# Performance work log

Hardware: AMD Instinct MI355X
Metric: run time of the kernel (lower is better)

The kernel has to match this reference:

```python
import jax, jax.numpy as jnp
import numpy as np

ALPHA = 0.2

def _ema_last_weights(T, alpha, dtype):
    # Closed form for the final EMA value after the sequential recurrence:
    # ema_T = (1-a)^(T-1) * x_0 + sum_{t=1}^{T-1} a*(1-a)^(T-1-t) * x_t
    t = jnp.arange(T)
    w = alpha * (1.0 - alpha) ** (T - 1 - t)
    w = w.at[0].set((1.0 - alpha) ** (T - 1))
    return w.astype(dtype)


def setup_inputs() -> dict:
    key = jax.random.key(0)
    k1, k2 = jax.random.split(key)
    B, T, F = 64, 2048, 256
    x = jax.random.normal(k1, (B, T, F), dtype=jnp.float32)
    W = jax.random.normal(k2, (F, F), dtype=jnp.float32) * (1.0 / np.sqrt(F))
    b = jnp.zeros((F,), dtype=jnp.float32)
    return {"x": x, "W": W, "b": b}


def reference(x, W, b):
    B, T, F = x.shape
    # final-step EMA over time (equivalent to the sequential python loop)
    w = _ema_last_weights(T, ALPHA, x.dtype)          # [T]
    last_ref = jnp.einsum('t,btf->bf', w, x)[:, None, :]  # [B,1,F]
    # base residual predictor: per-timestep linear
    res = jnp.einsum('btf,fg->btg', x, W) + b          # [B,T,F]
    return last_ref + res
```

## Files before the change

kernel.cpp:

```cpp
#include <hip/hip_runtime.h>

#define Bdim 64
#define Tdim 2048
#define Fdim 256
#define TAIL 256
#define NCH 8
#define CHT 32

#define NCHUNK 8
#define FR_STR 520

typedef __bf16 bf16x8 __attribute__((ext_vector_type(8)));
typedef float f32x16 __attribute__((ext_vector_type(16)));
typedef unsigned short u16x8 __attribute__((ext_vector_type(8)));

__device__ __forceinline__ unsigned short bf16_rne(float f) {
  unsigned int u = __float_as_uint(f);
  u += 0x7FFFu + ((u >> 16) & 1u);
  return (unsigned short)(u >> 16);
}

__global__ void prep(const float* __restrict__ x, const float* __restrict__ W,
                     unsigned short* __restrict__ Wf, float* __restrict__ part) {
  int blk = blockIdx.x;
  if (blk < Fdim) {
    int o = blk * 256 + threadIdx.x;
    int e = o & 7, lane = (o >> 3) & 63, wh = (o >> 9) & 1, s = (o >> 10) & 1;
    int c = (o >> 11) & 7, w = o >> 14;
    int n = w * 64 + wh * 32 + (lane & 31);
    int k = c * 32 + (2 * s + (lane >> 5)) * 8 + e;
    Wf[o] = bf16_rne(W[k * Fdim + n]);
  } else {
    int j = blk - Fdim;
    int b = j & 63, c = j >> 6;
    int f = threadIdx.x;
    int t0 = Tdim - TAIL + c * CHT;
    float w = 0.2f * exp2f((float)(Tdim - 1 - t0) * -0.32192809488736235f);
    const float* xp = x + ((size_t)b * Tdim + t0) * Fdim + f;
    float s = 0.f;
#pragma unroll
    for (int q = 0; q < CHT; ++q) {
      s += w * xp[(size_t)q * Fdim];
      w *= 1.25f;
    }
    part[(c * Bdim + b) * Fdim + f] = s;
  }
}

__global__ __launch_bounds__(256, 3)
void gemm_fused(const float* __restrict__ x, const unsigned short* __restrict__ Wf,
                const float* __restrict__ bias, const float* __restrict__ part,
                float* __restrict__ out) {
  __shared__ unsigned short Afrag[32 * FR_STR];
  __shared__ float lref[Fdim];

  const int tid = threadIdx.x;
  const int blk = blockIdx.x;
  const int b = blk >> 5;
  const size_t row0 = (size_t)blk * 64;

  const int wave = tid >> 6;
  const int lane = tid & 63;
  const int lm = lane & 31;
  const int half = lane >> 5;

  const int r = tid >> 2, q = tid & 3;
  const int iw = r >> 5;
  const int sq = q >> 1, hb = q & 1;
  const int dl = hb * 32 + (r & 31);
  const int wpos = dl ^ ((dl >> 5) << 2);
  const float* ap = x + (row0 + r) * Fdim + q * 8;

  float4 av[8][2];
#pragma unroll
  for (int p = 0; p < 8; ++p) {
    av[p][0] = *(const float4*)(ap + p * 32);
    av[p][1] = *(const float4*)(ap + p * 32 + 4);
  }

  {
    float s = bias[tid];
#pragma unroll
    for (int c = 0; c < NCH; ++c) s += part[(c * Bdim + b) * Fdim + tid];
    lref[tid] = s;
  }

#pragma unroll
  for (int p = 0; p < 8; ++p) {
    float4 v0 = av[p][0], v1 = av[p][1];
    u16x8 w;
    w[0] = bf16_rne(v0.x); w[1] = bf16_rne(v0.y);
    w[2] = bf16_rne(v0.z); w[3] = bf16_rne(v0.w);
    w[4] = bf16_rne(v1.x); w[5] = bf16_rne(v1.y);
    w[6] = bf16_rne(v1.z); w[7] = bf16_rne(v1.w);
    const int fragidx = (p * 2 + iw) * 2 + sq;
    *(u16x8*)&Afrag[fragidx * FR_STR + wpos * 8] = w;
  }
  __syncthreads();

  const unsigned short* bx = Wf + (size_t)wave * (32 * 512) + lane * 8;
  const int rpos = lane ^ ((lane >> 5) << 2);
  const unsigned short* abase = &Afrag[rpos * 8];

  f32x16 acc[2][2] = {};
  bf16x8 Bf[2][2][2];

#pragma unroll
  for (int cc = 0; cc < 2; ++cc)
#pragma unroll
    for (int s = 0; s < 2; ++s)
#pragma unroll
      for (int wh = 0; wh < 2; ++wh)
        Bf[cc][s][wh] = *(const bf16x8*)(bx + (size_t)(cc * 4 + s * 2 + wh) * 512);

#pragma unroll
  for (int c = 0; c < NCHUNK; ++c) {
    const int par = c & 1;
#pragma unroll
    for (int s = 0; s < 2; ++s) {
      bf16x8 a0 = *(const bf16x8*)&abase[((c * 2 + 0) * 2 + s) * FR_STR];
      bf16x8 a1 = *(const bf16x8*)&abase[((c * 2 + 1) * 2 + s) * FR_STR];
      acc[0][0] = __builtin_amdgcn_mfma_f32_32x32x16_bf16(a0, Bf[par][s][0], acc[0][0], 0, 0, 0);
      acc[0][1] = __builtin_amdgcn_mfma_f32_32x32x16_bf16(a0, Bf[par][s][1], acc[0][1], 0, 0, 0);
      acc[1][0] = __builtin_amdgcn_mfma_f32_32x32x16_bf16(a1, Bf[par][s][0], acc[1][0], 0, 0, 0);
      acc[1][1] = __builtin_amdgcn_mfma_f32_32x32x16_bf16(a1, Bf[par][s][1], acc[1][1], 0, 0, 0);
    }
    if (c + 2 < NCHUNK) {
#pragma unroll
      for (int s = 0; s < 2; ++s)
#pragma unroll
        for (int wh = 0; wh < 2; ++wh)
          Bf[par][s][wh] =
              *(const bf16x8*)(bx + (size_t)((c + 2) * 4 + s * 2 + wh) * 512);
    }
  }

  float* op = out + row0 * Fdim;
  const int rbase = 4 * half;
#pragma unroll
  for (int i = 0; i < 2; ++i) {
#pragma unroll
    for (int j = 0; j < 2; ++j) {
      int n = wave * 64 + j * 32 + lm;
      float lb = lref[n];
#pragma unroll
      for (int rr = 0; rr < 16; ++rr) {
        int rowi = i * 32 + (rr & 3) + 8 * (rr >> 2) + rbase;
        op[(size_t)rowi * Fdim + n] = acc[i][j][rr] + lb;
      }
    }
  }
}

extern "C" void kernel_launch(void* const* d_in, const int* in_sizes, int n_in,
                              void* d_out, int out_size, void* d_ws, size_t ws_size,
                              hipStream_t stream) {
  const float* x = (const float*)d_in[0];
  const float* W = (const float*)d_in[1];
  const float* bias = (const float*)d_in[2];
  float* out = (float*)d_out;

  unsigned short* Wf = (unsigned short*)d_ws;
  float* part = (float*)((char*)d_ws + Fdim * Fdim * sizeof(unsigned short));

  prep<<<Fdim + Bdim * NCH, 256, 0, stream>>>(x, W, Wf, part);
  gemm_fused<<<(Bdim * Tdim) / 64, 256, 0, stream>>>(x, Wf, bias, part, out);
}
```

Before: 243.1 us.

## Pre-convert x to bf16 MFMA fragments in prep and drop LDS staging

The bf16 conversion of x moves into the prep kernel, which writes it to workspace already in MFMA fragment order. The GEMM kernel then streams A fragments straight from global memory into registers with a 3-deep prefetch instead of staging them through shared memory. The wave tiling also changes from 1x4 to 2x2, so each wave computes 32 rows by 128 columns. The aim is to remove LDS traffic and the barrier wait on the A tile. The cost is an extra global round trip for x: an fp32 read plus a bf16 write in prep, then a bf16 read in the GEMM, and each wave now reads twice as much of W.

```diff
diff --git a/kernel.cpp b/kernel.cpp
--- a/kernel.cpp
+++ b/kernel.cpp
@@ -8,7 +8,7 @@
 #define CHT 32
 
 #define NCHUNK 8
-#define FR_STR 520
+#define AFD 3
 
 typedef __bf16 bf16x8 __attribute__((ext_vector_type(8)));
 typedef float f32x16 __attribute__((ext_vector_type(16)));
@@ -21,19 +21,21 @@
 }
 
 __global__ void prep(const float* __restrict__ x, const float* __restrict__ W,
-                     unsigned short* __restrict__ Wf, float* __restrict__ part) {
-  int blk = blockIdx.x;
+                     unsigned short* __restrict__ Wf, float* __restrict__ part,
+                     unsigned short* __restrict__ xf) {
+  const int blk = blockIdx.x;
+  const int tid = threadIdx.x;
   if (blk < Fdim) {
-    int o = blk * 256 + threadIdx.x;
+    int o = blk * 256 + tid;
     int e = o & 7, lane = (o >> 3) & 63, wh = (o >> 9) & 1, s = (o >> 10) & 1;
     int c = (o >> 11) & 7, w = o >> 14;
     int n = w * 64 + wh * 32 + (lane & 31);
     int k = c * 32 + (2 * s + (lane >> 5)) * 8 + e;
     Wf[o] = bf16_rne(W[k * Fdim + n]);
-  } else {
+  } else if (blk < Fdim + Bdim * NCH) {
     int j = blk - Fdim;
     int b = j & 63, c = j >> 6;
-    int f = threadIdx.x;
+    int f = tid;
     int t0 = Tdim - TAIL + c * CHT;
     float w = 0.2f * exp2f((float)(Tdim - 1 - t0) * -0.32192809488736235f);
     const float* xp = x + ((size_t)b * Tdim + t0) * Fdim + f;
@@ -44,39 +46,47 @@
       w *= 1.25f;
     }
     part[(c * Bdim + b) * Fdim + f] = s;
+  } else {
+    const int bb = blk - (Fdim + Bdim * NCH);
+    const int r = tid >> 2, q = tid & 3;
+    const float* ap = x + ((size_t)bb * 64 + r) * Fdim + q * 8;
+    float4 av[8][2];
+#pragma unroll
+    for (int p = 0; p < 8; ++p) {
+      av[p][0] = *(const float4*)(ap + p * 32);
+      av[p][1] = *(const float4*)(ap + p * 32 + 4);
+    }
+    const int mt = bb * 2 + (r >> 5);
+    const int rr = r & 31;
+#pragma unroll
+    for (int p = 0; p < 8; ++p) {
+      int g = p * 4 + q, c = g >> 2, s = (g >> 1) & 1, hb = g & 1;
+      float4 v0 = av[p][0], v1 = av[p][1];
+      u16x8 w;
+      w[0] = bf16_rne(v0.x); w[1] = bf16_rne(v0.y);
+      w[2] = bf16_rne(v0.z); w[3] = bf16_rne(v0.w);
+      w[4] = bf16_rne(v1.x); w[5] = bf16_rne(v1.y);
+      w[6] = bf16_rne(v1.z); w[7] = bf16_rne(v1.w);
+      *(u16x8*)&xf[((size_t)((mt * 16 + c * 2 + s) * 64 + hb * 32 + rr)) * 8] = w;
+    }
   }
 }
 
 __global__ __launch_bounds__(256, 3)
-void gemm_fused(const float* __restrict__ x, const unsigned short* __restrict__ Wf,
+void gemm_fused(const unsigned short* __restrict__ xf, const unsigned short* __restrict__ Wf,
                 const float* __restrict__ bias, const float* __restrict__ part,
                 float* __restrict__ out) {
-  __shared__ unsigned short Afrag[32 * FR_STR];
   __shared__ float lref[Fdim];
 
   const int tid = threadIdx.x;
   const int blk = blockIdx.x;
   const int b = blk >> 5;
-  const size_t row0 = (size_t)blk * 64;
-
   const int wave = tid >> 6;
+  const int mw = wave >> 1;
+  const int nw = wave & 1;
   const int lane = tid & 63;
   const int lm = lane & 31;
   const int half = lane >> 5;
-
-  const int r = tid >> 2, q = tid & 3;
-  const int iw = r >> 5;
-  const int sq = q >> 1, hb = q & 1;
-  const int dl = hb * 32 + (r & 31);
-  const int wpos = dl ^ ((dl >> 5) << 2);
-  const float* ap = x + (row0 + r) * Fdim + q * 8;
-
-  float4 av[8][2];
-#pragma unroll
-  for (int p = 0; p < 8; ++p) {
-    av[p][0] = *(const float4*)(ap + p * 32);
-    av[p][1] = *(const float4*)(ap + p * 32 + 4);
-  }
 
   {
     float s = bias[tid];
@@ -84,70 +94,67 @@
     for (int c = 0; c < NCH; ++c) s += part[(c * Bdim + b) * Fdim + tid];
     lref[tid] = s;
   }
+  __syncthreads();
+
+  const size_t mt = (size_t)blk * 2 + mw;
+  const unsigned short* ax = xf + mt * (16 * 512) + lane * 8;
+  const unsigned short* bx = Wf + lane * 8;
+
+#define BOFF(c, s, j) ((size_t)(((nw * 2 + ((j) >> 1)) * 32 + (c) * 4 + (s) * 2 + ((j) & 1))) * 512)
+
+  f32x16 acc[4] = {};
+  bf16x8 Af[AFD][2];
+  bf16x8 Bf[2][2][4];
 
 #pragma unroll
-  for (int p = 0; p < 8; ++p) {
-    float4 v0 = av[p][0], v1 = av[p][1];
-    u16x8 w;
-    w[0] = bf16_rne(v0.x); w[1] = bf16_rne(v0.y);
-    w[2] = bf16_rne(v0.z); w[3] = bf16_rne(v0.w);
-    w[4] = bf16_rne(v1.x); w[5] = bf16_rne(v1.y);
-    w[6] = bf16_rne(v1.z); w[7] = bf16_rne(v1.w);
-    const int fragidx = (p * 2 + iw) * 2 + sq;
-    *(u16x8*)&Afrag[fragidx * FR_STR + wpos * 8] = w;
-  }
-  __syncthreads();
-
-  const unsigned short* bx = Wf + (size_t)wave * (32 * 512) + lane * 8;
-  const int rpos = lane ^ ((lane >> 5) << 2);
-  const unsigned short* abase = &Afrag[rpos * 8];
-
-  f32x16 acc[2][2] = {};
-  bf16x8 Bf[2][2][2];
-
+  for (int p = 0; p < AFD; ++p)
+#pragma unroll
+    for (int s = 0; s < 2; ++s)
+      Af[p][s] = *(const bf16x8*)(ax + (size_t)(p * 2 + s) * 512);
 #pragma unroll
   for (int cc = 0; cc < 2; ++cc)
 #pragma unroll
     for (int s = 0; s < 2; ++s)
 #pragma unroll
-      for (int wh = 0; wh < 2; ++wh)
-        Bf[cc][s][wh] = *(const bf16x8*)(bx + (size_t)(cc * 4 + s * 2 + wh) * 512);
+      for (int j = 0; j < 4; ++j)
+        Bf[cc][s][j] = *(const bf16x8*)(bx + BOFF(cc, s, j));
 
 #pragma unroll
   for (int c = 0; c < NCHUNK; ++c) {
+    const int slot = c % AFD;
     const int par = c & 1;
 #pragma unroll
     for (int s = 0; s < 2; ++s) {
-      bf16x8 a0 = *(const bf16x8*)&abase[((c * 2 + 0) * 2 + s) * FR_STR];
-      bf16x8 a1 = *(const bf16x8*)&abase[((c * 2 + 1) * 2 + s) * FR_STR];
-      acc[0][0] = __builtin_amdgcn_mfma_f32_32x32x16_bf16(a0, Bf[par][s][0], acc[0][0], 0, 0, 0);
-      acc[0][1] = __builtin_amdgcn_mfma_f32_32x32x16_bf16(a0, Bf[par][s][1], acc[0][1], 0, 0, 0);
-      acc[1][0] = __builtin_amdgcn_mfma_f32_32x32x16_bf16(a1, Bf[par][s][0], acc[1][0], 0, 0, 0);
-      acc[1][1] = __builtin_amdgcn_mfma_f32_32x32x16_bf16(a1, Bf[par][s][1], acc[1][1], 0, 0, 0);
+      bf16x8 a = Af[slot][s];
+      acc[0] = __builtin_amdgcn_mfma_f32_32x32x16_bf16(a, Bf[par][s][0], acc[0], 0, 0, 0);
+      acc[1] = __builtin_amdgcn_mfma_f32_32x32x16_bf16(a, Bf[par][s][1], acc[1], 0, 0, 0);
+      acc[2] = __builtin_amdgcn_mfma_f32_32x32x16_bf16(a, Bf[par][s][2], acc[2], 0, 0, 0);
+      acc[3] = __builtin_amdgcn_mfma_f32_32x32x16_bf16(a, Bf[par][s][3], acc[3], 0, 0, 0);
+    }
+    if (c + AFD < NCHUNK) {
+#pragma unroll
+      for (int s = 0; s < 2; ++s)
+        Af[slot][s] = *(const bf16x8*)(ax + (size_t)((c + AFD) * 2 + s) * 512);
     }
     if (c + 2 < NCHUNK) {
 #pragma unroll
       for (int s = 0; s < 2; ++s)
 #pragma unroll
-        for (int wh = 0; wh < 2; ++wh)
-          Bf[par][s][wh] =
-              *(const bf16x8*)(bx + (size_t)((c + 2) * 4 + s * 2 + wh) * 512);
+        for (int j = 0; j < 4; ++j)
+          Bf[par][s][j] = *(const bf16x8*)(bx + BOFF(c + 2, s, j));
     }
   }
+#undef BOFF
 
-  float* op = out + row0 * Fdim;
+  float* op = out + mt * 32 * Fdim + nw * 128;
   const int rbase = 4 * half;
 #pragma unroll
-  for (int i = 0; i < 2; ++i) {
+  for (int j = 0; j < 4; ++j) {
+    float lb = lref[nw * 128 + j * 32 + lm];
 #pragma unroll
-    for (int j = 0; j < 2; ++j) {
-      int n = wave * 64 + j * 32 + lm;
-      float lb = lref[n];
-#pragma unroll
-      for (int rr = 0; rr < 16; ++rr) {
-        int rowi = i * 32 + (rr & 3) + 8 * (rr >> 2) + rbase;
-        op[(size_t)rowi * Fdim + n] = acc[i][j][rr] + lb;
-      }
+    for (int r = 0; r < 16; ++r) {
+      int rowi = (r & 3) + 8 * (r >> 2) + rbase;
+      op[(size_t)rowi * Fdim + j * 32 + lm] = acc[j][r] + lb;
     }
   }
 }
@@ -161,8 +168,9 @@
   float* out = (float*)d_out;
 
   unsigned short* Wf = (unsigned short*)d_ws;
-  float* part = (float*)((char*)d_ws + Fdim * Fdim * sizeof(unsigned short));
+  float* part = (float*)((char*)d_ws + 131072);
+  unsigned short* xf = (unsigned short*)((char*)d_ws + 131072 + 524288);
 
-  prep<<<Fdim + Bdim * NCH, 256, 0, stream>>>(x, W, Wf, part);
-  gemm_fused<<<(Bdim * Tdim) / 64, 256, 0, stream>>>(x, Wf, bias, part, out);
+  prep<<<Fdim + Bdim * NCH + 2048, 256, 0, stream>>>(x, W, Wf, part, xf);
+  gemm_fused<<<(Bdim * Tdim) / 64, 256, 0, stream>>>(xf, Wf, bias, part, out);
 }
```

New measurement: 275.6 us. 13.4% more time.

## Use 128-row tiles with 8 waves, each owning a 32-column slice

Applied to the files above, without the earlier changes.

The GEMM block grows from 64 to 128 rows and from 4 to 8 waves. Each wave now computes a 128x32 output slice (four 32x32 MFMA tiles sharing one B fragment) instead of 64x64. The per-column EMA+bias term is computed in registers rather than staged through shared memory, which removes that LDS array. The change halves the grid, doubles LDS per block and alters register pressure and occupancy. It also shifts the ratio of A to B fragment reuse.

```diff
diff --git a/kernel.cpp b/kernel.cpp
--- a/kernel.cpp
+++ b/kernel.cpp
@@ -22,9 +22,10 @@
 
 __global__ void prep(const float* __restrict__ x, const float* __restrict__ W,
                      unsigned short* __restrict__ Wf, float* __restrict__ part) {
-  int blk = blockIdx.x;
+  const int blk = blockIdx.x;
+  const int tid = threadIdx.x;
   if (blk < Fdim) {
-    int o = blk * 256 + threadIdx.x;
+    int o = blk * 256 + tid;
     int e = o & 7, lane = (o >> 3) & 63, wh = (o >> 9) & 1, s = (o >> 10) & 1;
     int c = (o >> 11) & 7, w = o >> 14;
     int n = w * 64 + wh * 32 + (lane & 31);
@@ -33,7 +34,7 @@
   } else {
     int j = blk - Fdim;
     int b = j & 63, c = j >> 6;
-    int f = threadIdx.x;
+    int f = tid;
     int t0 = Tdim - TAIL + c * CHT;
     float w = 0.2f * exp2f((float)(Tdim - 1 - t0) * -0.32192809488736235f);
     const float* xp = x + ((size_t)b * Tdim + t0) * Fdim + f;
@@ -47,107 +48,104 @@
   }
 }
 
-__global__ __launch_bounds__(256, 3)
+__global__ __launch_bounds__(512, 4)
 void gemm_fused(const float* __restrict__ x, const unsigned short* __restrict__ Wf,
                 const float* __restrict__ bias, const float* __restrict__ part,
                 float* __restrict__ out) {
-  __shared__ unsigned short Afrag[32 * FR_STR];
-  __shared__ float lref[Fdim];
+  __shared__ unsigned short Afrag[64 * FR_STR];
 
   const int tid = threadIdx.x;
   const int blk = blockIdx.x;
-  const int b = blk >> 5;
-  const size_t row0 = (size_t)blk * 64;
+  const int b = blk >> 4;
+  const size_t row0 = (size_t)blk * 128;
 
   const int wave = tid >> 6;
   const int lane = tid & 63;
   const int lm = lane & 31;
   const int half = lane >> 5;
+  const int w4 = wave >> 1;
+  const int wh = wave & 1;
+
+  const int ncol = wave * 32 + lm;
+  float lr = bias[ncol];
+#pragma unroll
+  for (int c = 0; c < NCH; ++c) lr += part[(c * Bdim + b) * Fdim + ncol];
 
   const int r = tid >> 2, q = tid & 3;
-  const int iw = r >> 5;
-  const int sq = q >> 1, hb = q & 1;
+  const int iw = r >> 5, sq = q >> 1, hb = q & 1;
   const int dl = hb * 32 + (r & 31);
   const int wpos = dl ^ ((dl >> 5) << 2);
   const float* ap = x + (row0 + r) * Fdim + q * 8;
 
-  float4 av[8][2];
 #pragma unroll
-  for (int p = 0; p < 8; ++p) {
-    av[p][0] = *(const float4*)(ap + p * 32);
-    av[p][1] = *(const float4*)(ap + p * 32 + 4);
-  }
-
-  {
-    float s = bias[tid];
+  for (int h = 0; h < 2; ++h) {
+    float4 av[4][2];
 #pragma unroll
-    for (int c = 0; c < NCH; ++c) s += part[(c * Bdim + b) * Fdim + tid];
-    lref[tid] = s;
-  }
-
+    for (int p4 = 0; p4 < 4; ++p4) {
+      const int p = h * 4 + p4;
+      av[p4][0] = *(const float4*)(ap + p * 32);
+      av[p4][1] = *(const float4*)(ap + p * 32 + 4);
+    }
 #pragma unroll
-  for (int p = 0; p < 8; ++p) {
-    float4 v0 = av[p][0], v1 = av[p][1];
-    u16x8 w;
-    w[0] = bf16_rne(v0.x); w[1] = bf16_rne(v0.y);
-    w[2] = bf16_rne(v0.z); w[3] = bf16_rne(v0.w);
-    w[4] = bf16_rne(v1.x); w[5] = bf16_rne(v1.y);
-    w[6] = bf16_rne(v1.z); w[7] = bf16_rne(v1.w);
-    const int fragidx = (p * 2 + iw) * 2 + sq;
-    *(u16x8*)&Afrag[fragidx * FR_STR + wpos * 8] = w;
+    for (int p4 = 0; p4 < 4; ++p4) {
+      const int p = h * 4 + p4;
+      float4 v0 = av[p4][0], v1 = av[p4][1];
+      u16x8 w;
+      w[0] = bf16_rne(v0.x); w[1] = bf16_rne(v0.y);
+      w[2] = bf16_rne(v0.z); w[3] = bf16_rne(v0.w);
+      w[4] = bf16_rne(v1.x); w[5] = bf16_rne(v1.y);
+      w[6] = bf16_rne(v1.z); w[7] = bf16_rne(v1.w);
+      const int fragidx = (p * 4 + iw) * 2 + sq;
+      *(u16x8*)&Afrag[fragidx * FR_STR + wpos * 8] = w;
+    }
   }
   __syncthreads();
 
-  const unsigned short* bx = Wf + (size_t)wave * (32 * 512) + lane * 8;
+  const unsigned short* bx = Wf + (size_t)w4 * (32 * 512) + lane * 8;
+#define BOFF(c, s) ((size_t)((c) * 4 + (s) * 2 + wh) * 512)
+
   const int rpos = lane ^ ((lane >> 5) << 2);
   const unsigned short* abase = &Afrag[rpos * 8];
 
-  f32x16 acc[2][2] = {};
-  bf16x8 Bf[2][2][2];
+  f32x16 acc[4] = {};
+  bf16x8 Bf[2][2];
 
 #pragma unroll
   for (int cc = 0; cc < 2; ++cc)
 #pragma unroll
     for (int s = 0; s < 2; ++s)
-#pragma unroll
-      for (int wh = 0; wh < 2; ++wh)
-        Bf[cc][s][wh] = *(const bf16x8*)(bx + (size_t)(cc * 4 + s * 2 + wh) * 512);
+      Bf[cc][s] = *(const bf16x8*)(bx + BOFF(cc, s));
 
 #pragma unroll
   for (int c = 0; c < NCHUNK; ++c) {
     const int par = c & 1;
 #pragma unroll
     for (int s = 0; s < 2; ++s) {
-      bf16x8 a0 = *(const bf16x8*)&abase[((c * 2 + 0) * 2 + s) * FR_STR];
-      bf16x8 a1 = *(const bf16x8*)&abase[((c * 2 + 1) * 2 + s) * FR_STR];
-      acc[0][0] = __builtin_amdgcn_mfma_f32_32x32x16_bf16(a0, Bf[par][s][0], acc[0][0], 0, 0, 0);
-      acc[0][1] = __builtin_amdgcn_mfma_f32_32x32x16_bf16(a0, Bf[par][s][1], acc[0][1], 0, 0, 0);
-      acc[1][0] = __builtin_amdgcn_mfma_f32_32x32x16_bf16(a1, Bf[par][s][0], acc[1][0], 0, 0, 0);
-      acc[1][1] = __builtin_amdgcn_mfma_f32_32x32x16_bf16(a1, Bf[par][s][1], acc[1][1], 0, 0, 0);
+      bf16x8 a0 = *(const bf16x8*)&abase[((c * 4 + 0) * 2 + s) * FR_STR];
+      bf16x8 a1 = *(const bf16x8*)&abase[((c * 4 + 1) * 2 + s) * FR_STR];
+      bf16x8 a2 = *(const bf16x8*)&abase[((c * 4 + 2) * 2 + s) * FR_STR];
+      bf16x8 a3 = *(const bf16x8*)&abase[((c * 4 + 3) * 2 + s) * FR_STR];
+      acc[0] = __builtin_amdgcn_mfma_f32_32x32x16_bf16(a0, Bf[par][s], acc[0], 0, 0, 0);
+      acc[1] = __builtin_amdgcn_mfma_f32_32x32x16_bf16(a1, Bf[par][s], acc[1], 0, 0, 0);
+      acc[2] = __builtin_amdgcn_mfma_f32_32x32x16_bf16(a2, Bf[par][s], acc[2], 0, 0, 0);
+      acc[3] = __builtin_amdgcn_mfma_f32_32x32x16_bf16(a3, Bf[par][s], acc[3], 0, 0, 0);
     }
     if (c + 2 < NCHUNK) {
 #pragma unroll
       for (int s = 0; s < 2; ++s)
-#pragma unroll
-        for (int wh = 0; wh < 2; ++wh)
-          Bf[par][s][wh] =
-              *(const bf16x8*)(bx + (size_t)((c + 2) * 4 + s * 2 + wh) * 512);
+        Bf[par][s] = *(const bf16x8*)(bx + BOFF(c + 2, s));
     }
   }
+#undef BOFF
 
-  float* op = out + row0 * Fdim;
+  float* op = out + row0 * Fdim + ncol;
   const int rbase = 4 * half;
 #pragma unroll
-  for (int i = 0; i < 2; ++i) {
+  for (int i = 0; i < 4; ++i) {
 #pragma unroll
-    for (int j = 0; j < 2; ++j) {
-      int n = wave * 64 + j * 32 + lm;
-      float lb = lref[n];
-#pragma unroll
-      for (int rr = 0; rr < 16; ++rr) {
-        int rowi = i * 32 + (rr & 3) + 8 * (rr >> 2) + rbase;
-        op[(size_t)rowi * Fdim + n] = acc[i][j][rr] + lb;
-      }
+    for (int rr = 0; rr < 16; ++rr) {
+      const int rowi = i * 32 + (rr & 3) + 8 * (rr >> 2) + rbase;
+      op[(size_t)rowi * Fdim] = acc[i][rr] + lr;
     }
   }
 }
@@ -161,8 +159,8 @@
   float* out = (float*)d_out;
 
   unsigned short* Wf = (unsigned short*)d_ws;
-  float* part = (float*)((char*)d_ws + Fdim * Fdim * sizeof(unsigned short));
+  float* part = (float*)((char*)d_ws + 131072);
 
   prep<<<Fdim + Bdim * NCH, 256, 0, stream>>>(x, W, Wf, part);
-  gemm_fused<<<(Bdim * Tdim) / 64, 256, 0, stream>>>(x, Wf, bias, part, out);
+  gemm_fused<<<(Bdim * Tdim) / 128, 512, 0, stream>>>(x, Wf, bias, part, out);
 }
```

Measured after the change: 245.9 us. About the same (+1.1%).
